# Performance work log

Hardware: AMD Instinct MI355X
Metric: run time of the kernel (lower is better)

Reference implementation:

```python
import jax, jax.numpy as jnp
import numpy as np

NUM_CHANNELS = 256
NUM_HEADS = 8
HEAD_DIM = NUM_CHANNELS // NUM_HEADS


def setup_inputs() -> dict:
    key = jax.random.key(0)
    k1, k2, k3, k4, k5 = jax.random.split(key, 5)
    C = NUM_CHANNELS
    s = 1.0 / np.sqrt(C)
    image = jax.random.normal(k1, (8, C, 32, 32), dtype=jnp.float32)
    # kqv_projection: Linear(C, 3C); mix_heads: Linear(C, C). Stored as [in, out].
    w_kqv = jax.random.uniform(k2, (C, 3 * C), minval=-s, maxval=s, dtype=jnp.float32)
    b_kqv = jax.random.uniform(k3, (3 * C,), minval=-s, maxval=s, dtype=jnp.float32)
    w_mix = jax.random.uniform(k4, (C, C), minval=-s, maxval=s, dtype=jnp.float32)
    b_mix = jax.random.uniform(k5, (C,), minval=-s, maxval=s, dtype=jnp.float32)
    return {"image": image, "w_kqv": w_kqv, "b_kqv": b_kqv, "w_mix": w_mix, "b_mix": b_mix}


def _masked_attention(seq, w_kqv, b_kqv, w_mix, b_mix):
    # seq: [N, T, C]
    N, T, C = seq.shape
    H, D = NUM_HEADS, HEAD_DIM
    projected = seq @ w_kqv + b_kqv            # [N, T, 3C]
    k, q, v = jnp.split(projected, 3, axis=-1)  # order: keys, queries, values
    # split heads -> [N, H, T, D]
    k = k.reshape(N, T, H, D).transpose(0, 2, 1, 3)
    q = q.reshape(N, T, H, D).transpose(0, 2, 1, 3)
    v = v.reshape(N, T, H, D).transpose(0, 2, 1, 3)
    logits = jnp.einsum('nhtd,nhsd->nhts', q, k) / jnp.sqrt(jnp.float32(D))
    causal = jnp.tril(jnp.ones((T, T), dtype=bool))
    logits = jnp.where(causal, logits, -jnp.inf)
    weights = jax.nn.softmax(logits, axis=-1)
    out = jnp.einsum('nhts,nhsd->nhtd', weights, v)  # [N, H, T, D]
    out = out.transpose(0, 2, 1, 3).reshape(N, T, C)  # combine heads
    return out @ w_mix + b_mix


def reference(image, w_kqv, b_kqv, w_mix, b_mix):
    N, C, Hh, Ww = image.shape
    seq = image.transpose(0, 2, 3, 1).reshape(N, Hh * Ww, C)
    attn = _masked_attention(seq, w_kqv, b_kqv, w_mix, b_mix)
    attn = attn.reshape(N, Hh, Ww, C).transpose(0, 3, 1, 2)
    return attn + image
```

## Files before the change

### kernel.cpp

```cpp
#include <hip/hip_runtime.h>
#include <math.h>

constexpr int NB  = 8;
constexpr int C   = 256;
constexpr int T   = 1024;
constexpr int NH  = 8;
constexpr int HD  = 32;
constexpr int C3  = 768;

constexpr float QSCALE = 0.25503489422229562f;

typedef __attribute__((ext_vector_type(8))) short bf16x8;
typedef __attribute__((ext_vector_type(4))) float f32x4;

__device__ inline short f2bf(float f) {
    unsigned u = __float_as_uint(f);
    u += 0x7FFF + ((u >> 16) & 1);
    return (short)(u >> 16);
}
__device__ inline short f2bf_trunc(float f) {
    return (short)(__float_as_uint(f) >> 16);
}

__global__ __launch_bounds__(256) void kqv_mfma(const float* __restrict__ image,
                                                const float* __restrict__ wkqv,
                                                const float* __restrict__ bkqv,
                                                short* __restrict__ Kb,
                                                short* __restrict__ Qb,
                                                short* __restrict__ Vb) {
    __shared__ __align__(16) short As[128][40];
    __shared__ __align__(16) short Bs[64][40];
    const int tid = threadIdx.x;
    const int n0 = blockIdx.x * 64;
    const int m0 = blockIdx.y * 128;
    const int nb = m0 >> 10, t0 = m0 & 1023;
    const int wv = tid >> 6, lane = tid & 63;
    const int m = lane & 15, quad = lane >> 4;
    const int am = tid & 63, ak8 = (tid >> 6) * 8;

    const float* imgn = image + (size_t)nb * C * T;

    f32x4 acc[2][4];
    const f32x4 z = {0.f, 0.f, 0.f, 0.f};
    #pragma unroll
    for (int i = 0; i < 2; ++i)
        #pragma unroll
        for (int j = 0; j < 4; ++j) acc[i][j] = z;

    float fa[2][8], fb[8];
    #pragma unroll
    for (int i = 0; i < 8; ++i) {
        fa[0][i] = imgn[(size_t)(ak8 + i) * T + t0 + am];
        fa[1][i] = imgn[(size_t)(ak8 + i) * T + t0 + 64 + am];
        fb[i]    = wkqv[(size_t)(ak8 + i) * C3 + n0 + am];
    }

    for (int k0 = 0; k0 < C; k0 += 32) {
        __syncthreads();
        #pragma unroll
        for (int h2 = 0; h2 < 2; ++h2) {
            short4 lo = { f2bf(fa[h2][0]), f2bf(fa[h2][1]), f2bf(fa[h2][2]), f2bf(fa[h2][3]) };
            short4 hi = { f2bf(fa[h2][4]), f2bf(fa[h2][5]), f2bf(fa[h2][6]), f2bf(fa[h2][7]) };
            *(short4*)&As[64 * h2 + am][ak8]     = lo;
            *(short4*)&As[64 * h2 + am][ak8 + 4] = hi;
        }
        {
            short4 lo = { f2bf(fb[0]), f2bf(fb[1]), f2bf(fb[2]), f2bf(fb[3]) };
            short4 hi = { f2bf(fb[4]), f2bf(fb[5]), f2bf(fb[6]), f2bf(fb[7]) };
            *(short4*)&Bs[am][ak8]     = lo;
            *(short4*)&Bs[am][ak8 + 4] = hi;
        }
        if (k0 + 32 < C) {
            #pragma unroll
            for (int i = 0; i < 8; ++i) {
                fa[0][i] = imgn[(size_t)(k0 + 32 + ak8 + i) * T + t0 + am];
                fa[1][i] = imgn[(size_t)(k0 + 32 + ak8 + i) * T + t0 + 64 + am];
                fb[i]    = wkqv[(size_t)(k0 + 32 + ak8 + i) * C3 + n0 + am];
            }
        }
        __syncthreads();
        bf16x8 a[2], b[4];
        #pragma unroll
        for (int i = 0; i < 2; ++i) a[i] = *(const bf16x8*)&As[32 * wv + 16 * i + m][8 * quad];
        #pragma unroll
        for (int j = 0; j < 4; ++j) b[j] = *(const bf16x8*)&Bs[16 * j + m][8 * quad];
        #pragma unroll
        for (int i = 0; i < 2; ++i)
            #pragma unroll
            for (int j = 0; j < 4; ++j)
                acc[i][j] = __builtin_amdgcn_mfma_f32_16x16x32_bf16(a[i], b[j], acc[i][j], 0, 0, 0);
    }

    #pragma unroll
    for (int j = 0; j < 4; ++j) {
        int jj = n0 + 16 * j + m;
        int chunk = jj >> 8, hh = (jj >> 5) & 7, d = jj & 31;
        short* dst = (chunk == 0) ? Kb : (chunk == 1) ? Qb : Vb;
        float bias = bkqv[jj];
        float mul = (chunk == 1) ? QSCALE : 1.0f;
        size_t base = (size_t)(nb * NH + hh) * T * HD + d;
        #pragma unroll
        for (int i = 0; i < 2; ++i) {
            int t = t0 + 32 * wv + 16 * i + 4 * quad;
            #pragma unroll
            for (int r = 0; r < 4; ++r)
                dst[base + (size_t)(t + r) * HD] = f2bf((acc[i][j][r] + bias) * mul);
        }
    }
}

__global__ __launch_bounds__(256) void attn_mfma(const short* __restrict__ Kb,
                                                 const short* __restrict__ Qb,
                                                 const short* __restrict__ Vb,
                                                 short* __restrict__ attnb) {
    const int qp = blockIdx.x;
    const int h  = blockIdx.y;
    const int nb = blockIdx.z;
    const int tid  = threadIdx.x;
    const int wv   = tid >> 6;
    const int lane = tid & 63;
    const int m    = lane & 15;
    const int quad = lane >> 4;

    __shared__ __align__(16) short Qs[128][40];
    __shared__ __align__(16) short Ks[2][64][40];
    __shared__ __align__(16) short Vt[2][32][72];
    __shared__ __align__(16) short Ps[128][72];

    const size_t hb = (size_t)(nb * NH + h) * T * HD;
    const short* Kp = Kb + hb;
    const short* Qp = Qb + hb;
    const short* Vp = Vb + hb;
    const int sr = tid >> 2, sc8 = (tid & 3) * 8;
    const f32x4 z = {0.f, 0.f, 0.f, 0.f};

    #pragma unroll 1
    for (int pp = 0; pp < 2; ++pp) {
        const int qb  = pp ? 7 - qp : qp;
        const int q0  = qb * 128;
        const int nst = 2 * qb + 2;

        __syncthreads();

        *(bf16x8*)&Qs[sr][sc8]      = *(const bf16x8*)&Qp[(size_t)(q0 + sr) * HD + sc8];
        *(bf16x8*)&Qs[64 + sr][sc8] = *(const bf16x8*)&Qp[(size_t)(q0 + 64 + sr) * HD + sc8];
        bf16x8 kreg = *(const bf16x8*)&Kp[(size_t)sr * HD + sc8];
        bf16x8 vreg = *(const bf16x8*)&Vp[(size_t)sr * HD + sc8];
        *(bf16x8*)&Ks[0][sr][sc8] = kreg;
        #pragma unroll
        for (int i2 = 0; i2 < 8; ++i2) Vt[0][sc8 + i2][sr] = vreg[i2];

        f32x4 O[2][2] = {{z, z}, {z, z}};
        float lp[2][4] = {};

        for (int st = 0; st < nst; ++st) {
            const int p = st & 1;
            __syncthreads();
            if (st + 1 < nst) {
                kreg = *(const bf16x8*)&Kp[(size_t)((st + 1) * 64 + sr) * HD + sc8];
                vreg = *(const bf16x8*)&Vp[(size_t)((st + 1) * 64 + sr) * HD + sc8];
            }

            bf16x8 bk[4];
            #pragma unroll
            for (int j = 0; j < 4; ++j) bk[j] = *(const bf16x8*)&Ks[p][16 * j + m][8 * quad];
            f32x4 S[2][4];
            #pragma unroll
            for (int i = 0; i < 2; ++i) {
                bf16x8 aq = *(const bf16x8*)&Qs[32 * wv + 16 * i + m][8 * quad];
                #pragma unroll
                for (int j = 0; j < 4; ++j)
                    S[i][j] = __builtin_amdgcn_mfma_f32_16x16x32_bf16(aq, bk[j], z, 0, 0, 0);
            }

            const bool msk = (st >= 2 * qb);
            const int s0 = st * 64;
            #pragma unroll
            for (int i = 0; i < 2; ++i) {
                const int qr_base = q0 + 32 * wv + 16 * i + 4 * quad;
                #pragma unroll
                for (int j = 0; j < 4; ++j) {
                    const int sc = s0 + 16 * j + m;
                    #pragma unroll
                    for (int r = 0; r < 4; ++r) {
                        float e = __builtin_amdgcn_exp2f(S[i][j][r]);
                        if (msk && sc > qr_base + r) e = 0.f;
                        lp[i][r] += e;
                        Ps[32 * wv + 16 * i + 4 * quad + r][16 * j + m] = f2bf_trunc(e);
                    }
                }
            }

            #pragma unroll
            for (int kc = 0; kc < 2; ++kc) {
                bf16x8 ap0 = *(const bf16x8*)&Ps[32 * wv + m][32 * kc + 8 * quad];
                bf16x8 ap1 = *(const bf16x8*)&Ps[32 * wv + 16 + m][32 * kc + 8 * quad];
                bf16x8 b0  = *(const bf16x8*)&Vt[p][m][32 * kc + 8 * quad];
                bf16x8 b1  = *(const bf16x8*)&Vt[p][16 + m][32 * kc + 8 * quad];
                O[0][0] = __builtin_amdgcn_mfma_f32_16x16x32_bf16(ap0, b0, O[0][0], 0, 0, 0);
                O[0][1] = __builtin_amdgcn_mfma_f32_16x16x32_bf16(ap0, b1, O[0][1], 0, 0, 0);
                O[1][0] = __builtin_amdgcn_mfma_f32_16x16x32_bf16(ap1, b0, O[1][0], 0, 0, 0);
                O[1][1] = __builtin_amdgcn_mfma_f32_16x16x32_bf16(ap1, b1, O[1][1], 0, 0, 0);
            }

            if (st + 1 < nst) {
                const int pn = p ^ 1;
                *(bf16x8*)&Ks[pn][sr][sc8] = kreg;
                #pragma unroll
                for (int i2 = 0; i2 < 8; ++i2) Vt[pn][sc8 + i2][sr] = vreg[i2];
            }
        }

        #pragma unroll
        for (int i = 0; i < 2; ++i)
            #pragma unroll
            for (int r = 0; r < 4; ++r) {
                float l = lp[i][r];
                l += __shfl_xor(l, 1);
                l += __shfl_xor(l, 2);
                l += __shfl_xor(l, 4);
                l += __shfl_xor(l, 8);
                float inv = 1.f / l;
                int row = q0 + 32 * wv + 16 * i + 4 * quad + r;
                short* op = attnb + ((size_t)(nb * T + row)) * C + h * HD;
                op[m]      = f2bf(O[i][0][r] * inv);
                op[16 + m] = f2bf(O[i][1][r] * inv);
            }
    }
}

__global__ __launch_bounds__(256) void mix_mfma(const short* __restrict__ attnb,
                                                const float* __restrict__ wmix,
                                                const float* __restrict__ bmix,
                                                const float* __restrict__ image,
                                                float* __restrict__ out) {
    __shared__ __align__(16) short As[64][40];
    __shared__ __align__(16) short Bs[64][40];
    const int tid = threadIdx.x;
    const int n0 = blockIdx.x * 64;
    const int m0 = blockIdx.y * 64;
    const int nb = m0 >> 10, t0 = m0 & 1023;
    const int wv = tid >> 6, lane = tid & 63;
    const int m = lane & 15, quad = lane >> 4;
    const int sr = tid >> 2, sc8 = (tid & 3) * 8;
    const int am = tid & 63, ak8 = (tid >> 6) * 8;

    f32x4 acc[4];
    const f32x4 z = {0.f, 0.f, 0.f, 0.f};
    #pragma unroll
    for (int j = 0; j < 4; ++j) acc[j] = z;

    bf16x8 areg = *(const bf16x8*)&attnb[(size_t)(m0 + sr) * C + sc8];
    float fb[8];
    #pragma unroll
    for (int i = 0; i < 8; ++i)
        fb[i] = wmix[(size_t)(ak8 + i) * C + n0 + am];

    for (int k0 = 0; k0 < C; k0 += 32) {
        __syncthreads();
        *(bf16x8*)&As[sr][sc8] = areg;
        {
            short4 lo = { f2bf(fb[0]), f2bf(fb[1]), f2bf(fb[2]), f2bf(fb[3]) };
            short4 hi = { f2bf(fb[4]), f2bf(fb[5]), f2bf(fb[6]), f2bf(fb[7]) };
            *(short4*)&Bs[am][ak8]     = lo;
            *(short4*)&Bs[am][ak8 + 4] = hi;
        }
        if (k0 + 32 < C) {
            areg = *(const bf16x8*)&attnb[(size_t)(m0 + sr) * C + k0 + 32 + sc8];
            #pragma unroll
            for (int i = 0; i < 8; ++i)
                fb[i] = wmix[(size_t)(k0 + 32 + ak8 + i) * C + n0 + am];
        }
        __syncthreads();
        bf16x8 a = *(const bf16x8*)&As[16 * wv + m][8 * quad];
        bf16x8 b[4];
        #pragma unroll
        for (int j = 0; j < 4; ++j) b[j] = *(const bf16x8*)&Bs[16 * j + m][8 * quad];
        #pragma unroll
        for (int j = 0; j < 4; ++j)
            acc[j] = __builtin_amdgcn_mfma_f32_16x16x32_bf16(a, b[j], acc[j], 0, 0, 0);
    }

    const int tb = t0 + 16 * wv + 4 * quad;
    #pragma unroll
    for (int j = 0; j < 4; ++j) {
        int c = n0 + 16 * j + m;
        float bias = bmix[c];
        size_t o = (size_t)(nb * C + c) * T + tb;
        float4 img = *(const float4*)&image[o];
        float4 res = { acc[j][0] + bias + img.x,
                       acc[j][1] + bias + img.y,
                       acc[j][2] + bias + img.z,
                       acc[j][3] + bias + img.w };
        *(float4*)&out[o] = res;
    }
}

extern "C" void kernel_launch(void* const* d_in, const int* in_sizes, int n_in,
                              void* d_out, int out_size, void* d_ws, size_t ws_size,
                              hipStream_t stream) {
    const float* image = (const float*)d_in[0];
    const float* w_kqv = (const float*)d_in[1];
    const float* b_kqv = (const float*)d_in[2];
    const float* w_mix = (const float*)d_in[3];
    const float* b_mix = (const float*)d_in[4];
    float* out = (float*)d_out;

    short* Kb    = (short*)d_ws;
    short* Qb    = Kb + (size_t)NB * NH * T * HD;
    short* Vb    = Qb + (size_t)NB * NH * T * HD;
    short* attnb = Vb + (size_t)NB * NH * T * HD;

    kqv_mfma<<<dim3(C3 / 64, NB * T / 128), 256, 0, stream>>>(image, w_kqv, b_kqv, Kb, Qb, Vb);
    attn_mfma<<<dim3(4, NH, NB), 256, 0, stream>>>(Kb, Qb, Vb, attnb);
    mix_mfma<<<dim3(C / 64, NB * T / 64), 256, 0, stream>>>(attnb, w_mix, b_mix, image, out);
}
```

Baseline: 111.7 us.

## Pre-transpose V tiles, load K/Q/V from global into registers, stage full w_mix

The projection kernel now writes V in a pre-transposed, 64-token-tiled layout. This lets the attention kernel load Q, K and V fragments straight from global memory into MFMA registers, with no LDS staging, no per-step barriers and no scalar V transpose. Attention launches one block per query tile (8x more blocks) instead of pairing two tiles per block, and mirrors the tile order for half the batches to keep load balanced. The mix kernel converts all of its w_mix columns into LDS once and reads attention rows directly from global memory, which removes the per-k barriers. The trade-off is more redundant global and L2 traffic, since K and V are reloaded per wave, plus scattered 2-byte stores when writing the V layout.

```diff
diff --git a/kernel.cpp b/kernel.cpp
--- a/kernel.cpp
+++ b/kernel.cpp
@@ -27,7 +27,7 @@
                                                 const float* __restrict__ bkqv,
                                                 short* __restrict__ Kb,
                                                 short* __restrict__ Qb,
-                                                short* __restrict__ Vb) {
+                                                short* __restrict__ Vtb) {
     __shared__ __align__(16) short As[128][40];
     __shared__ __align__(16) short Bs[64][40];
     const int tid = threadIdx.x;
@@ -95,25 +95,37 @@
     for (int j = 0; j < 4; ++j) {
         int jj = n0 + 16 * j + m;
         int chunk = jj >> 8, hh = (jj >> 5) & 7, d = jj & 31;
-        short* dst = (chunk == 0) ? Kb : (chunk == 1) ? Qb : Vb;
         float bias = bkqv[jj];
-        float mul = (chunk == 1) ? QSCALE : 1.0f;
-        size_t base = (size_t)(nb * NH + hh) * T * HD + d;
-        #pragma unroll
-        for (int i = 0; i < 2; ++i) {
-            int t = t0 + 32 * wv + 16 * i + 4 * quad;
-            #pragma unroll
-            for (int r = 0; r < 4; ++r)
-                dst[base + (size_t)(t + r) * HD] = f2bf((acc[i][j][r] + bias) * mul);
+        if (chunk < 2) {
+            short* dst = (chunk == 0) ? Kb : Qb;
+            float mul = (chunk == 1) ? QSCALE : 1.0f;
+            size_t base = (size_t)(nb * NH + hh) * T * HD + d;
+            #pragma unroll
+            for (int i = 0; i < 2; ++i) {
+                int t = t0 + 32 * wv + 16 * i + 4 * quad;
+                #pragma unroll
+                for (int r = 0; r < 4; ++r)
+                    dst[base + (size_t)(t + r) * HD] = f2bf((acc[i][j][r] + bias) * mul);
+            }
+        } else {
+            size_t base = (size_t)(nb * NH + hh) * (16 * 2048) + (size_t)d * 64;
+            #pragma unroll
+            for (int i = 0; i < 2; ++i) {
+                #pragma unroll
+                for (int r = 0; r < 4; ++r) {
+                    int t = t0 + 32 * wv + 16 * i + 4 * quad + r;
+                    Vtb[base + (size_t)(t >> 6) * 2048 + (t & 63)] = f2bf(acc[i][j][r] + bias);
+                }
+            }
         }
     }
 }
 
 __global__ __launch_bounds__(256) void attn_mfma(const short* __restrict__ Kb,
                                                  const short* __restrict__ Qb,
-                                                 const short* __restrict__ Vb,
+                                                 const short* __restrict__ Vtb,
                                                  short* __restrict__ attnb) {
-    const int qp = blockIdx.x;
+    const int qb = (blockIdx.z & 4) ? 7 - blockIdx.x : blockIdx.x;
     const int h  = blockIdx.y;
     const int nb = blockIdx.z;
     const int tid  = threadIdx.x;
@@ -122,111 +134,101 @@
     const int m    = lane & 15;
     const int quad = lane >> 4;
 
-    __shared__ __align__(16) short Qs[128][40];
-    __shared__ __align__(16) short Ks[2][64][40];
-    __shared__ __align__(16) short Vt[2][32][72];
     __shared__ __align__(16) short Ps[128][72];
 
+    const int q0  = qb * 128;
+    const int nst = 2 * qb + 2;
     const size_t hb = (size_t)(nb * NH + h) * T * HD;
     const short* Kp = Kb + hb;
     const short* Qp = Qb + hb;
-    const short* Vp = Vb + hb;
-    const int sr = tid >> 2, sc8 = (tid & 3) * 8;
+    const short* Vp = Vtb + (size_t)(nb * NH + h) * (16 * 2048);
     const f32x4 z = {0.f, 0.f, 0.f, 0.f};
 
-    #pragma unroll 1
-    for (int pp = 0; pp < 2; ++pp) {
-        const int qb  = pp ? 7 - qp : qp;
-        const int q0  = qb * 128;
-        const int nst = 2 * qb + 2;
-
-        __syncthreads();
-
-        *(bf16x8*)&Qs[sr][sc8]      = *(const bf16x8*)&Qp[(size_t)(q0 + sr) * HD + sc8];
-        *(bf16x8*)&Qs[64 + sr][sc8] = *(const bf16x8*)&Qp[(size_t)(q0 + 64 + sr) * HD + sc8];
-        bf16x8 kreg = *(const bf16x8*)&Kp[(size_t)sr * HD + sc8];
-        bf16x8 vreg = *(const bf16x8*)&Vp[(size_t)sr * HD + sc8];
-        *(bf16x8*)&Ks[0][sr][sc8] = kreg;
-        #pragma unroll
-        for (int i2 = 0; i2 < 8; ++i2) Vt[0][sc8 + i2][sr] = vreg[i2];
-
-        f32x4 O[2][2] = {{z, z}, {z, z}};
-        float lp[2][4] = {};
-
-        for (int st = 0; st < nst; ++st) {
-            const int p = st & 1;
-            __syncthreads();
-            if (st + 1 < nst) {
-                kreg = *(const bf16x8*)&Kp[(size_t)((st + 1) * 64 + sr) * HD + sc8];
-                vreg = *(const bf16x8*)&Vp[(size_t)((st + 1) * 64 + sr) * HD + sc8];
-            }
-
-            bf16x8 bk[4];
-            #pragma unroll
-            for (int j = 0; j < 4; ++j) bk[j] = *(const bf16x8*)&Ks[p][16 * j + m][8 * quad];
-            f32x4 S[2][4];
-            #pragma unroll
-            for (int i = 0; i < 2; ++i) {
-                bf16x8 aq = *(const bf16x8*)&Qs[32 * wv + 16 * i + m][8 * quad];
+    bf16x8 aq[2];
+    #pragma unroll
+    for (int i = 0; i < 2; ++i)
+        aq[i] = *(const bf16x8*)&Qp[(size_t)(q0 + 32 * wv + 16 * i + m) * HD + 8 * quad];
+
+    bf16x8 bk[4], vb[2][2];
+    #pragma unroll
+    for (int j = 0; j < 4; ++j)
+        bk[j] = *(const bf16x8*)&Kp[(size_t)(16 * j + m) * HD + 8 * quad];
+    #pragma unroll
+    for (int kc = 0; kc < 2; ++kc)
+        #pragma unroll
+        for (int hf = 0; hf < 2; ++hf)
+            vb[kc][hf] = *(const bf16x8*)&Vp[(size_t)(16 * hf + m) * 64 + 32 * kc + 8 * quad];
+
+    f32x4 O[2][2] = {{z, z}, {z, z}};
+    float lp[2][4] = {};
+
+    for (int st = 0; st < nst; ++st) {
+        f32x4 S[2][4];
+        #pragma unroll
+        for (int i = 0; i < 2; ++i)
+            #pragma unroll
+            for (int j = 0; j < 4; ++j)
+                S[i][j] = __builtin_amdgcn_mfma_f32_16x16x32_bf16(aq[i], bk[j], z, 0, 0, 0);
+
+        if (st + 1 < nst) {
+            #pragma unroll
+            for (int j = 0; j < 4; ++j)
+                bk[j] = *(const bf16x8*)&Kp[(size_t)((st + 1) * 64 + 16 * j + m) * HD + 8 * quad];
+        }
+
+        const bool msk = (st >= 2 * qb);
+        const int s0 = st * 64;
+        #pragma unroll
+        for (int i = 0; i < 2; ++i) {
+            const int qr_base = q0 + 32 * wv + 16 * i + 4 * quad;
+            #pragma unroll
+            for (int j = 0; j < 4; ++j) {
+                const int sc = s0 + 16 * j + m;
                 #pragma unroll
-                for (int j = 0; j < 4; ++j)
-                    S[i][j] = __builtin_amdgcn_mfma_f32_16x16x32_bf16(aq, bk[j], z, 0, 0, 0);
-            }
-
-            const bool msk = (st >= 2 * qb);
-            const int s0 = st * 64;
-            #pragma unroll
-            for (int i = 0; i < 2; ++i) {
-                const int qr_base = q0 + 32 * wv + 16 * i + 4 * quad;
-                #pragma unroll
-                for (int j = 0; j < 4; ++j) {
-                    const int sc = s0 + 16 * j + m;
-                    #pragma unroll
-                    for (int r = 0; r < 4; ++r) {
-                        float e = __builtin_amdgcn_exp2f(S[i][j][r]);
-                        if (msk && sc > qr_base + r) e = 0.f;
-                        lp[i][r] += e;
-                        Ps[32 * wv + 16 * i + 4 * quad + r][16 * j + m] = f2bf_trunc(e);
-                    }
+                for (int r = 0; r < 4; ++r) {
+                    float e = __builtin_amdgcn_exp2f(S[i][j][r]);
+                    if (msk && sc > qr_base + r) e = 0.f;
+                    lp[i][r] += e;
+                    Ps[32 * wv + 16 * i + 4 * quad + r][16 * j + m] = f2bf_trunc(e);
                 }
             }
-
-            #pragma unroll
-            for (int kc = 0; kc < 2; ++kc) {
-                bf16x8 ap0 = *(const bf16x8*)&Ps[32 * wv + m][32 * kc + 8 * quad];
-                bf16x8 ap1 = *(const bf16x8*)&Ps[32 * wv + 16 + m][32 * kc + 8 * quad];
-                bf16x8 b0  = *(const bf16x8*)&Vt[p][m][32 * kc + 8 * quad];
-                bf16x8 b1  = *(const bf16x8*)&Vt[p][16 + m][32 * kc + 8 * quad];
-                O[0][0] = __builtin_amdgcn_mfma_f32_16x16x32_bf16(ap0, b0, O[0][0], 0, 0, 0);
-                O[0][1] = __builtin_amdgcn_mfma_f32_16x16x32_bf16(ap0, b1, O[0][1], 0, 0, 0);
-                O[1][0] = __builtin_amdgcn_mfma_f32_16x16x32_bf16(ap1, b0, O[1][0], 0, 0, 0);
-                O[1][1] = __builtin_amdgcn_mfma_f32_16x16x32_bf16(ap1, b1, O[1][1], 0, 0, 0);
-            }
-
-            if (st + 1 < nst) {
-                const int pn = p ^ 1;
-                *(bf16x8*)&Ks[pn][sr][sc8] = kreg;
+        }
+
+        #pragma unroll
+        for (int kc = 0; kc < 2; ++kc) {
+            bf16x8 ap0 = *(const bf16x8*)&Ps[32 * wv + m][32 * kc + 8 * quad];
+            bf16x8 ap1 = *(const bf16x8*)&Ps[32 * wv + 16 + m][32 * kc + 8 * quad];
+            O[0][0] = __builtin_amdgcn_mfma_f32_16x16x32_bf16(ap0, vb[kc][0], O[0][0], 0, 0, 0);
+            O[0][1] = __builtin_amdgcn_mfma_f32_16x16x32_bf16(ap0, vb[kc][1], O[0][1], 0, 0, 0);
+            O[1][0] = __builtin_amdgcn_mfma_f32_16x16x32_bf16(ap1, vb[kc][0], O[1][0], 0, 0, 0);
+            O[1][1] = __builtin_amdgcn_mfma_f32_16x16x32_bf16(ap1, vb[kc][1], O[1][1], 0, 0, 0);
+        }
+
+        if (st + 1 < nst) {
+            const short* Vn = Vp + (size_t)(st + 1) * 2048;
+            #pragma unroll
+            for (int kc = 0; kc < 2; ++kc)
                 #pragma unroll
-                for (int i2 = 0; i2 < 8; ++i2) Vt[pn][sc8 + i2][sr] = vreg[i2];
-            }
-        }
-
-        #pragma unroll
-        for (int i = 0; i < 2; ++i)
-            #pragma unroll
-            for (int r = 0; r < 4; ++r) {
-                float l = lp[i][r];
-                l += __shfl_xor(l, 1);
-                l += __shfl_xor(l, 2);
-                l += __shfl_xor(l, 4);
-                l += __shfl_xor(l, 8);
-                float inv = 1.f / l;
-                int row = q0 + 32 * wv + 16 * i + 4 * quad + r;
-                short* op = attnb + ((size_t)(nb * T + row)) * C + h * HD;
-                op[m]      = f2bf(O[i][0][r] * inv);
-                op[16 + m] = f2bf(O[i][1][r] * inv);
-            }
-    }
+                for (int hf = 0; hf < 2; ++hf)
+                    vb[kc][hf] = *(const bf16x8*)&Vn[(size_t)(16 * hf + m) * 64 + 32 * kc + 8 * quad];
+        }
+    }
+
+    #pragma unroll
+    for (int i = 0; i < 2; ++i)
+        #pragma unroll
+        for (int r = 0; r < 4; ++r) {
+            float l = lp[i][r];
+            l += __shfl_xor(l, 1);
+            l += __shfl_xor(l, 2);
+            l += __shfl_xor(l, 4);
+            l += __shfl_xor(l, 8);
+            float inv = 1.f / l;
+            int row = q0 + 32 * wv + 16 * i + 4 * quad + r;
+            short* op = attnb + ((size_t)(nb * T + row)) * C + h * HD;
+            op[m]      = f2bf(O[i][0][r] * inv);
+            op[16 + m] = f2bf(O[i][1][r] * inv);
+        }
 }
 
 __global__ __launch_bounds__(256) void mix_mfma(const short* __restrict__ attnb,
@@ -234,48 +236,40 @@
                                                 const float* __restrict__ bmix,
                                                 const float* __restrict__ image,
                                                 float* __restrict__ out) {
-    __shared__ __align__(16) short As[64][40];
-    __shared__ __align__(16) short Bs[64][40];
+    __shared__ __align__(16) short Bs[64][264];
     const int tid = threadIdx.x;
     const int n0 = blockIdx.x * 64;
     const int m0 = blockIdx.y * 64;
     const int nb = m0 >> 10, t0 = m0 & 1023;
     const int wv = tid >> 6, lane = tid & 63;
     const int m = lane & 15, quad = lane >> 4;
-    const int sr = tid >> 2, sc8 = (tid & 3) * 8;
-    const int am = tid & 63, ak8 = (tid >> 6) * 8;
+    const int bn = tid & 63, bk8 = (tid >> 6) * 8;
+
+    #pragma unroll
+    for (int g = 0; g < 8; ++g) {
+        int kk = bk8 + 32 * g;
+        float fb[8];
+        #pragma unroll
+        for (int i = 0; i < 8; ++i)
+            fb[i] = wmix[(size_t)(kk + i) * C + n0 + bn];
+        short4 lo = { f2bf(fb[0]), f2bf(fb[1]), f2bf(fb[2]), f2bf(fb[3]) };
+        short4 hi = { f2bf(fb[4]), f2bf(fb[5]), f2bf(fb[6]), f2bf(fb[7]) };
+        *(short4*)&Bs[bn][kk]     = lo;
+        *(short4*)&Bs[bn][kk + 4] = hi;
+    }
+    __syncthreads();
 
     f32x4 acc[4];
     const f32x4 z = {0.f, 0.f, 0.f, 0.f};
     #pragma unroll
     for (int j = 0; j < 4; ++j) acc[j] = z;
 
-    bf16x8 areg = *(const bf16x8*)&attnb[(size_t)(m0 + sr) * C + sc8];
-    float fb[8];
-    #pragma unroll
-    for (int i = 0; i < 8; ++i)
-        fb[i] = wmix[(size_t)(ak8 + i) * C + n0 + am];
-
+    #pragma unroll
     for (int k0 = 0; k0 < C; k0 += 32) {
-        __syncthreads();
-        *(bf16x8*)&As[sr][sc8] = areg;
-        {
-            short4 lo = { f2bf(fb[0]), f2bf(fb[1]), f2bf(fb[2]), f2bf(fb[3]) };
-            short4 hi = { f2bf(fb[4]), f2bf(fb[5]), f2bf(fb[6]), f2bf(fb[7]) };
-            *(short4*)&Bs[am][ak8]     = lo;
-            *(short4*)&Bs[am][ak8 + 4] = hi;
-        }
-        if (k0 + 32 < C) {
-            areg = *(const bf16x8*)&attnb[(size_t)(m0 + sr) * C + k0 + 32 + sc8];
-            #pragma unroll
-            for (int i = 0; i < 8; ++i)
-                fb[i] = wmix[(size_t)(k0 + 32 + ak8 + i) * C + n0 + am];
-        }
-        __syncthreads();
-        bf16x8 a = *(const bf16x8*)&As[16 * wv + m][8 * quad];
+        bf16x8 a = *(const bf16x8*)&attnb[(size_t)(m0 + 16 * wv + m) * C + k0 + 8 * quad];
         bf16x8 b[4];
         #pragma unroll
-        for (int j = 0; j < 4; ++j) b[j] = *(const bf16x8*)&Bs[16 * j + m][8 * quad];
+        for (int j = 0; j < 4; ++j) b[j] = *(const bf16x8*)&Bs[16 * j + m][k0 + 8 * quad];
         #pragma unroll
         for (int j = 0; j < 4; ++j)
             acc[j] = __builtin_amdgcn_mfma_f32_16x16x32_bf16(a, b[j], acc[j], 0, 0, 0);
@@ -307,11 +301,11 @@
     float* out = (float*)d_out;
 
     short* Kb    = (short*)d_ws;
-    short* Qb    = Kb + (size_t)NB * NH * T * HD;
-    short* Vb    = Qb + (size_t)NB * NH * T * HD;
-    short* attnb = Vb + (size_t)NB * NH * T * HD;
-
-    kqv_mfma<<<dim3(C3 / 64, NB * T / 128), 256, 0, stream>>>(image, w_kqv, b_kqv, Kb, Qb, Vb);
-    attn_mfma<<<dim3(4, NH, NB), 256, 0, stream>>>(Kb, Qb, Vb, attnb);
+    short* Qb    = Kb  + (size_t)NB * NH * T * HD;
+    short* Vtb   = Qb  + (size_t)NB * NH * T * HD;
+    short* attnb = Vtb + (size_t)NB * NH * T * HD;
+
+    kqv_mfma<<<dim3(C3 / 64, NB * T / 128), 256, 0, stream>>>(image, w_kqv, b_kqv, Kb, Qb, Vtb);
+    attn_mfma<<<dim3(8, NH, NB), 256, 0, stream>>>(Kb, Qb, Vtb, attnb);
     mix_mfma<<<dim3(C / 64, NB * T / 64), 256, 0, stream>>>(attnb, w_mix, b_mix, image, out);
 }
```

New measurement: 108.5 us. -2.9%, faster.
